# Performance work log

Hardware: AMD Instinct MI355X
Metric: run time of the kernel (lower is better)

The kernel has to match this reference:

```python
import jax, jax.numpy as jnp
import numpy as np

TAGSET = 64
START_TAG = 62
STOP_TAG = 63
B, S = 32, 256


def setup_inputs() -> dict:
    key = jax.random.key(0)
    k1, k2, k3 = jax.random.split(key, 3)
    features = jax.random.normal(k1, (B, S, TAGSET, TAGSET), dtype=jnp.float32)
    targets = jax.random.randint(k2, (B, S), 0, TAGSET * TAGSET, dtype=jnp.int64)
    lengths = jax.random.randint(k3, (B,), 1, S + 1, dtype=jnp.int64)
    # pack_padded_sequence requires lengths sorted descending; ensure max length = S
    lengths = jnp.sort(lengths)[::-1].at[0].set(S)
    return {"features": features, "targets": targets, "lengths": lengths}


def reference(features, targets, lengths):
    Bc, Sc, T, _ = features.shape
    # --- gold score: gather the score of the true (from_tag, to_tag) pair per token ---
    flat = features.reshape(Bc, Sc, T * T)                       # [B,S,T*T]
    scores_at_targets = jnp.take_along_axis(flat, targets[:, :, None], axis=2)[..., 0]
    valid = (jnp.arange(Sc)[None, :] < lengths[:, None])          # [B,S] pad mask
    gold_score = jnp.sum(jnp.where(valid, scores_at_targets, 0.0))

    # --- CRF forward algorithm (log-sum-exp recurrence over time) ---
    init = features[:, 0, START_TAG, :]                           # [B,T] (all lengths >= 1)
    feats_t = jnp.swapaxes(features, 0, 1)[1:]                    # [S-1,B,T,T]
    active = (jnp.arange(1, Sc)[:, None] < lengths[None, :])       # [S-1,B]

    def step(scores, inp):
        feat, act = inp                                           # feat [B,T,T], act [B]
        new = jax.nn.logsumexp(feat + scores[:, :, None], axis=1)  # lse over from-tag
        scores = jnp.where(act[:, None], new, scores)
        return scores, None

    scores_upto_t, _ = jax.lax.scan(step, init, (feats_t, active))
    all_paths_scores = jnp.sum(scores_upto_t[:, STOP_TAG])

    return (all_paths_scores - gold_score) / Bc
```

## Files before the change

### kernel.cpp

```cpp
#include <hip/hip_runtime.h>
#include <cmath>

#define NB 32
#define NS 256
#define NT 64
#define START_TAG 62
#define STOP_TAG 63
#define CL 8
#define NCH 32
#define GS 8.0f
#define LOG64 4.1588830833596715f
#define SP 66

typedef __attribute__((ext_vector_type(8))) short short8;
typedef __attribute__((ext_vector_type(4))) float float4v;

union FragU { unsigned u[4]; short8 s; };

__device__ inline unsigned short f2bf(float x) {
  unsigned u = __float_as_uint(x);
  u += 0x7fffu + ((u >> 16) & 1u);
  return (unsigned short)(u >> 16);
}
__device__ inline unsigned pack2(float a, float b) {
  return (unsigned)f2bf(a) | ((unsigned)f2bf(b) << 16);
}

__global__ __launch_bounds__(256) void chunk_kernel(
    const float* __restrict__ feat, const int* __restrict__ lengths,
    unsigned int* __restrict__ cmat) {
  const int b = blockIdx.x;
  const int c = blockIdx.y;
  const int len = lengths[b];
  const int t1 = 1 + c * CL;
  const int nmat = min(len, t1 + CL) - t1;
  if (nmat <= 0) return;

  __shared__ unsigned short Pb[2][NT * SP];
  __shared__ unsigned short Et[2][NT * SP];

  const int tid = threadIdx.x;
  const float* fb = feat + ((size_t)b * NS + t1) * (NT * NT);

  {
    const int cj = tid & 15, rk = tid >> 4;
    #pragma unroll
    for (int r = 0; r < 4; ++r) {
      const int row = rk + 16 * r;
      float4 f4 = *(const float4*)(fb + row * NT + 4 * cj);
      unsigned* dst = (unsigned*)&Pb[0][row * SP + 4 * cj];
      dst[0] = pack2(__expf(f4.x - GS), __expf(f4.y - GS));
      dst[1] = pack2(__expf(f4.z - GS), __expf(f4.w - GS));
    }
  }

  const int sj = tid & 15, r0 = tid >> 4;
  float4 raw[2][4];
  if (nmat > 1) {
    const float* p = fb + (NT * NT);
    raw[1][0] = *(const float4*)(p + (2 * r0     ) * NT + 4 * sj);
    raw[1][1] = *(const float4*)(p + (2 * r0 +  1) * NT + 4 * sj);
    raw[1][2] = *(const float4*)(p + (2 * r0 + 32) * NT + 4 * sj);
    raw[1][3] = *(const float4*)(p + (2 * r0 + 33) * NT + 4 * sj);
  }
  __syncthreads();

  const int lane = tid & 63, wv = tid >> 6;
  const int ln = lane & 15, q = lane >> 4;
  const int m0 = 16 * wv;
  int pp = 0;

  for (int k = 1; k < nmat; ++k) {
    const int pf = k & 1;
    if (k + 1 < nmat) {
      const float* p = fb + (size_t)(k + 1) * (NT * NT);
      raw[1 - pf][0] = *(const float4*)(p + (2 * r0     ) * NT + 4 * sj);
      raw[1 - pf][1] = *(const float4*)(p + (2 * r0 +  1) * NT + 4 * sj);
      raw[1 - pf][2] = *(const float4*)(p + (2 * r0 + 32) * NT + 4 * sj);
      raw[1 - pf][3] = *(const float4*)(p + (2 * r0 + 33) * NT + 4 * sj);
    }
    {
      unsigned short* et = Et[pf];
      const float* r0p = (const float*)&raw[pf][0];
      const float* r1p = (const float*)&raw[pf][1];
      const float* r2p = (const float*)&raw[pf][2];
      const float* r3p = (const float*)&raw[pf][3];
      #pragma unroll
      for (int cc = 0; cc < 4; ++cc) {
        const int j = 4 * sj + cc;
        *(unsigned*)&et[j * SP + 2 * r0] =
            pack2(__expf(r0p[cc] - GS), __expf(r1p[cc] - GS));
        *(unsigned*)&et[j * SP + 2 * r0 + 32] =
            pack2(__expf(r2p[cc] - GS), __expf(r3p[cc] - GS));
      }
    }
    __syncthreads();

    FragU a0, a1;
    const unsigned* ap = (const unsigned*)&Pb[pp][(m0 + ln) * SP];
    a0.u[0] = ap[4 * q + 0]; a0.u[1] = ap[4 * q + 1];
    a0.u[2] = ap[4 * q + 2]; a0.u[3] = ap[4 * q + 3];
    a1.u[0] = ap[16 + 4 * q + 0]; a1.u[1] = ap[16 + 4 * q + 1];
    a1.u[2] = ap[16 + 4 * q + 2]; a1.u[3] = ap[16 + 4 * q + 3];

    float4v acc[4];
    #pragma unroll
    for (int tc = 0; tc < 4; ++tc) {
      FragU b0, b1;
      const unsigned* bp = (const unsigned*)&Et[pf][(16 * tc + ln) * SP];
      b0.u[0] = bp[4 * q + 0]; b0.u[1] = bp[4 * q + 1];
      b0.u[2] = bp[4 * q + 2]; b0.u[3] = bp[4 * q + 3];
      b1.u[0] = bp[16 + 4 * q + 0]; b1.u[1] = bp[16 + 4 * q + 1];
      b1.u[2] = bp[16 + 4 * q + 2]; b1.u[3] = bp[16 + 4 * q + 3];
      float4v z = {0.f, 0.f, 0.f, 0.f};
      acc[tc] = __builtin_amdgcn_mfma_f32_16x16x32_bf16(a0.s, b0.s, z, 0, 0, 0);
      acc[tc] = __builtin_amdgcn_mfma_f32_16x16x32_bf16(a1.s, b1.s, acc[tc], 0, 0, 0);
    }

    unsigned short* pn = Pb[1 - pp];
    #pragma unroll
    for (int tc = 0; tc < 4; ++tc) {
      #pragma unroll
      for (int rg = 0; rg < 4; ++rg) {
        const int row = m0 + 4 * q + rg;
        pn[row * SP + 16 * tc + ln] = f2bf(acc[tc][rg] * 0.015625f);
      }
    }
    pp ^= 1;
  }
  __syncthreads();

  {
    const int j = tid >> 2, cg = tid & 3;
    unsigned ub[8];
    #pragma unroll
    for (int u = 0; u < 8; ++u) {
      unsigned short lo = Pb[pp][(16 * cg + 2 * u    ) * SP + j];
      unsigned short hi = Pb[pp][(16 * cg + 2 * u + 1) * SP + j];
      ub[u] = (unsigned)lo | ((unsigned)hi << 16);
    }
    unsigned* dst = cmat + ((size_t)b * NCH + c) * 2048 + j * 32 + cg * 8;
    *(uint4*)dst       = make_uint4(ub[0], ub[1], ub[2], ub[3]);
    *((uint4*)dst + 1) = make_uint4(ub[4], ub[5], ub[6], ub[7]);
  }
}

__global__ __launch_bounds__(64) void combine_kernel(
    const float* __restrict__ feat, const int* __restrict__ targets,
    const int* __restrict__ lengths, const unsigned int* __restrict__ cmat,
    float* __restrict__ out) {
  const int b = blockIdx.x;
  const int j = threadIdx.x;
  __shared__ float sv[NT];
  const int len = lengths[b];
  const float* f0 = feat + (size_t)b * NS * (NT * NT);

  float gold = 0.f;
  #pragma unroll
  for (int g = 0; g < 4; ++g) {
    const int s = j + 64 * g;
    if (s < len) {
      const int tgt = targets[b * NS + s];
      gold += f0[(size_t)s * (NT * NT) + tgt];
    }
  }

  float x = f0[START_TAG * NT + j];
  float m = x;
  #pragma unroll
  for (int off = 32; off; off >>= 1) m = fmaxf(m, __shfl_xor(m, off));
  float v = __expf(x - m);
  float L = m;

  const int nch = (len - 1 + CL - 1) / CL;
  uint4 Q0[8];
  if (nch > 0) {
    const uint4* P = (const uint4*)cmat + (size_t)b * NCH * 512 + j * 8;
    #pragma unroll
    for (int w = 0; w < 8; ++w) Q0[w] = P[w];
  }

  for (int c2 = 0; c2 < nch; ++c2) {
    sv[j] = v;
    __builtin_amdgcn_wave_barrier();

    uint4 Q1[8];
    if (c2 + 1 < nch) {
      const uint4* P = (const uint4*)cmat + ((size_t)b * NCH + c2 + 1) * 512 + j * 8;
      #pragma unroll
      for (int w = 0; w < 8; ++w) Q1[w] = P[w];
    }

    float acc = 0.f;
    const float4* svp = (const float4*)sv;
    #pragma unroll
    for (int w = 0; w < 8; ++w) {
      uint4 qq = Q0[w];
      float4 s0 = svp[2 * w], s1 = svp[2 * w + 1];
      acc = fmaf(__uint_as_float(qq.x << 16), s0.x, acc);
      acc = fmaf(__uint_as_float(qq.x & 0xffff0000u), s0.y, acc);
      acc = fmaf(__uint_as_float(qq.y << 16), s0.z, acc);
      acc = fmaf(__uint_as_float(qq.y & 0xffff0000u), s0.w, acc);
      acc = fmaf(__uint_as_float(qq.z << 16), s1.x, acc);
      acc = fmaf(__uint_as_float(qq.z & 0xffff0000u), s1.y, acc);
      acc = fmaf(__uint_as_float(qq.w << 16), s1.z, acc);
      acc = fmaf(__uint_as_float(qq.w & 0xffff0000u), s1.w, acc);
    }
    __builtin_amdgcn_wave_barrier();

    const int tt1 = 1 + c2 * CL;
    const int nmat = min(len, tt1 + CL) - tt1;
    L += (float)nmat * GS + (float)(nmat - 1) * LOG64;

    float mm = acc;
    #pragma unroll
    for (int off = 32; off; off >>= 1) mm = fmaxf(mm, __shfl_xor(mm, off));
    v = acc / mm;
    L += __logf(mm);

    #pragma unroll
    for (int w = 0; w < 8; ++w) Q0[w] = Q1[w];
  }

  float lv = __logf(v);
  float path = L + __shfl(lv, STOP_TAG);

  #pragma unroll
  for (int off = 32; off; off >>= 1) gold += __shfl_down(gold, off);
  if (j == 0) atomicAdd(out, (path - gold) * (1.0f / (float)NB));
}

extern "C" void kernel_launch(void* const* d_in, const int* in_sizes, int n_in,
                              void* d_out, int out_size, void* d_ws, size_t ws_size,
                              hipStream_t stream) {
  const float* feat    = (const float*)d_in[0];
  const int*   targets = (const int*)d_in[1];
  const int*   lengths = (const int*)d_in[2];
  unsigned int* cmat = (unsigned int*)d_ws;
  float* out = (float*)d_out;

  hipMemsetAsync(d_out, 0, sizeof(float), stream);
  chunk_kernel<<<dim3(NB, NCH), 256, 0, stream>>>(feat, lengths, cmat);
  combine_kernel<<<NB, 64, 0, stream>>>(feat, targets, lengths, cmat, out);
}
```

Before: 240.9 us.

## Compute each chunk product in one wave with register-resident MFMA fragments

Each chunk of the CRF transfer-matrix product now runs on a single 64-lane wave instead of a 256-thread block. The running product stays in MFMA B-fragment registers and is re-laid out with lane shuffles, which removes the shared-memory staging and block-wide barriers. Incoming feature tiles are read with strided scalar loads straight into A-fragment order, and the 1/64 scale is folded into the exponent. The combine kernel's dot product is split over four independent accumulators to shorten the FMA dependency chain. The costs are uncoalesced global loads, many shuffles, higher register pressure, and a simpler round-to-nearest bf16 conversion that no longer breaks ties to even.

```diff
diff --git a/kernel.cpp b/kernel.cpp
--- a/kernel.cpp
+++ b/kernel.cpp
@@ -10,139 +10,135 @@
 #define NCH 32
 #define GS 8.0f
 #define LOG64 4.1588830833596715f
-#define SP 66
 
 typedef __attribute__((ext_vector_type(8))) short short8;
 typedef __attribute__((ext_vector_type(4))) float float4v;
 
-union FragU { unsigned u[4]; short8 s; };
-
-__device__ inline unsigned short f2bf(float x) {
-  unsigned u = __float_as_uint(x);
-  u += 0x7fffu + ((u >> 16) & 1u);
-  return (unsigned short)(u >> 16);
-}
-__device__ inline unsigned pack2(float a, float b) {
-  return (unsigned)f2bf(a) | ((unsigned)f2bf(b) << 16);
+union FragU { unsigned u[4]; short8 s; unsigned short h[8]; };
+
+__device__ inline unsigned pkbf(float a, float b) {
+  unsigned ua = (__float_as_uint(a) + 0x8000u) >> 16;
+  unsigned ub = (__float_as_uint(b) + 0x8000u) & 0xffff0000u;
+  return ua | ub;
 }
 
 __global__ __launch_bounds__(256) void chunk_kernel(
     const float* __restrict__ feat, const int* __restrict__ lengths,
-    unsigned int* __restrict__ cmat) {
-  const int b = blockIdx.x;
-  const int c = blockIdx.y;
+    unsigned short* __restrict__ cmat) {
+  const int wv  = threadIdx.x >> 6;
+  const int gid = blockIdx.x * 4 + wv;
+  const int b   = gid >> 5;
+  const int c   = gid & 31;
   const int len = lengths[b];
-  const int t1 = 1 + c * CL;
+  const int t1  = 1 + c * CL;
   const int nmat = min(len, t1 + CL) - t1;
   if (nmat <= 0) return;
 
-  __shared__ unsigned short Pb[2][NT * SP];
-  __shared__ unsigned short Et[2][NT * SP];
-
-  const int tid = threadIdx.x;
+  const int lane = threadIdx.x & 63;
+  const int q  = lane >> 4;
+  const int cc = lane & 15;
+
   const float* fb = feat + ((size_t)b * NS + t1) * (NT * NT);
 
-  {
-    const int cj = tid & 15, rk = tid >> 4;
-    #pragma unroll
-    for (int r = 0; r < 4; ++r) {
-      const int row = rk + 16 * r;
-      float4 f4 = *(const float4*)(fb + row * NT + 4 * cj);
-      unsigned* dst = (unsigned*)&Pb[0][row * SP + 4 * cj];
-      dst[0] = pack2(__expf(f4.x - GS), __expf(f4.y - GS));
-      dst[1] = pack2(__expf(f4.z - GS), __expf(f4.w - GS));
-    }
-  }
-
-  const int sj = tid & 15, r0 = tid >> 4;
-  float4 raw[2][4];
+  FragU BQ[2][4];
+  #pragma unroll
+  for (int h = 0; h < 2; ++h)
+    #pragma unroll
+    for (int tj = 0; tj < 4; ++tj) {
+      const float* p = fb + (16 * tj + cc) * NT + 32 * h + 8 * q;
+      float4 x = *(const float4*)p;
+      float4 y = *(const float4*)(p + 4);
+      BQ[h][tj].u[0] = pkbf(__expf(x.x - GS), __expf(x.y - GS));
+      BQ[h][tj].u[1] = pkbf(__expf(x.z - GS), __expf(x.w - GS));
+      BQ[h][tj].u[2] = pkbf(__expf(y.x - GS), __expf(y.y - GS));
+      BQ[h][tj].u[3] = pkbf(__expf(y.z - GS), __expf(y.w - GS));
+    }
+
+  float raw[4][2][8];
   if (nmat > 1) {
-    const float* p = fb + (NT * NT);
-    raw[1][0] = *(const float4*)(p + (2 * r0     ) * NT + 4 * sj);
-    raw[1][1] = *(const float4*)(p + (2 * r0 +  1) * NT + 4 * sj);
-    raw[1][2] = *(const float4*)(p + (2 * r0 + 32) * NT + 4 * sj);
-    raw[1][3] = *(const float4*)(p + (2 * r0 + 33) * NT + 4 * sj);
-  }
-  __syncthreads();
-
-  const int lane = tid & 63, wv = tid >> 6;
-  const int ln = lane & 15, q = lane >> 4;
-  const int m0 = 16 * wv;
-  int pp = 0;
+    const float* p = fb + NT * NT;
+    #pragma unroll
+    for (int mi = 0; mi < 4; ++mi)
+      #pragma unroll
+      for (int kh = 0; kh < 2; ++kh)
+        #pragma unroll
+        for (int j = 0; j < 8; ++j)
+          raw[mi][kh][j] = p[(32 * kh + 8 * q + j) * NT + 16 * mi + cc];
+  }
+
+  const int src0 = (((q & 1) * 2) << 4) | cc;
+  const int src1 = src0 + 16;
+  const bool hi = (q >> 1) != 0;
 
   for (int k = 1; k < nmat; ++k) {
-    const int pf = k & 1;
+    FragU FA[4][2];
+    #pragma unroll
+    for (int mi = 0; mi < 4; ++mi)
+      #pragma unroll
+      for (int kh = 0; kh < 2; ++kh)
+        #pragma unroll
+        for (int j2 = 0; j2 < 4; ++j2)
+          FA[mi][kh].u[j2] =
+              pkbf(__expf(raw[mi][kh][2 * j2]     - (GS + LOG64)),
+                   __expf(raw[mi][kh][2 * j2 + 1] - (GS + LOG64)));
+
     if (k + 1 < nmat) {
       const float* p = fb + (size_t)(k + 1) * (NT * NT);
-      raw[1 - pf][0] = *(const float4*)(p + (2 * r0     ) * NT + 4 * sj);
-      raw[1 - pf][1] = *(const float4*)(p + (2 * r0 +  1) * NT + 4 * sj);
-      raw[1 - pf][2] = *(const float4*)(p + (2 * r0 + 32) * NT + 4 * sj);
-      raw[1 - pf][3] = *(const float4*)(p + (2 * r0 + 33) * NT + 4 * sj);
-    }
-    {
-      unsigned short* et = Et[pf];
-      const float* r0p = (const float*)&raw[pf][0];
-      const float* r1p = (const float*)&raw[pf][1];
-      const float* r2p = (const float*)&raw[pf][2];
-      const float* r3p = (const float*)&raw[pf][3];
-      #pragma unroll
-      for (int cc = 0; cc < 4; ++cc) {
-        const int j = 4 * sj + cc;
-        *(unsigned*)&et[j * SP + 2 * r0] =
-            pack2(__expf(r0p[cc] - GS), __expf(r1p[cc] - GS));
-        *(unsigned*)&et[j * SP + 2 * r0 + 32] =
-            pack2(__expf(r2p[cc] - GS), __expf(r3p[cc] - GS));
+      #pragma unroll
+      for (int mi = 0; mi < 4; ++mi)
+        #pragma unroll
+        for (int kh = 0; kh < 2; ++kh)
+          #pragma unroll
+          for (int j = 0; j < 8; ++j)
+            raw[mi][kh][j] = p[(32 * kh + 8 * q + j) * NT + 16 * mi + cc];
+    }
+
+    float4v acc[4][4];
+    #pragma unroll
+    for (int ti = 0; ti < 4; ++ti)
+      #pragma unroll
+      for (int tj = 0; tj < 4; ++tj) {
+        float4v z = {0.f, 0.f, 0.f, 0.f};
+        z = __builtin_amdgcn_mfma_f32_16x16x32_bf16(FA[ti][0].s, BQ[0][tj].s, z, 0, 0, 0);
+        acc[ti][tj] = __builtin_amdgcn_mfma_f32_16x16x32_bf16(FA[ti][1].s, BQ[1][tj].s, z, 0, 0, 0);
       }
-    }
-    __syncthreads();
-
-    FragU a0, a1;
-    const unsigned* ap = (const unsigned*)&Pb[pp][(m0 + ln) * SP];
-    a0.u[0] = ap[4 * q + 0]; a0.u[1] = ap[4 * q + 1];
-    a0.u[2] = ap[4 * q + 2]; a0.u[3] = ap[4 * q + 3];
-    a1.u[0] = ap[16 + 4 * q + 0]; a1.u[1] = ap[16 + 4 * q + 1];
-    a1.u[2] = ap[16 + 4 * q + 2]; a1.u[3] = ap[16 + 4 * q + 3];
-
-    float4v acc[4];
-    #pragma unroll
-    for (int tc = 0; tc < 4; ++tc) {
-      FragU b0, b1;
-      const unsigned* bp = (const unsigned*)&Et[pf][(16 * tc + ln) * SP];
-      b0.u[0] = bp[4 * q + 0]; b0.u[1] = bp[4 * q + 1];
-      b0.u[2] = bp[4 * q + 2]; b0.u[3] = bp[4 * q + 3];
-      b1.u[0] = bp[16 + 4 * q + 0]; b1.u[1] = bp[16 + 4 * q + 1];
-      b1.u[2] = bp[16 + 4 * q + 2]; b1.u[3] = bp[16 + 4 * q + 3];
-      float4v z = {0.f, 0.f, 0.f, 0.f};
-      acc[tc] = __builtin_amdgcn_mfma_f32_16x16x32_bf16(a0.s, b0.s, z, 0, 0, 0);
-      acc[tc] = __builtin_amdgcn_mfma_f32_16x16x32_bf16(a1.s, b1.s, acc[tc], 0, 0, 0);
-    }
-
-    unsigned short* pn = Pb[1 - pp];
-    #pragma unroll
-    for (int tc = 0; tc < 4; ++tc) {
-      #pragma unroll
-      for (int rg = 0; rg < 4; ++rg) {
-        const int row = m0 + 4 * q + rg;
-        pn[row * SP + 16 * tc + ln] = f2bf(acc[tc][rg] * 0.015625f);
+
+    unsigned pk01[4][4], pk23[4][4];
+    #pragma unroll
+    for (int ti = 0; ti < 4; ++ti)
+      #pragma unroll
+      for (int tj = 0; tj < 4; ++tj) {
+        pk01[ti][tj] = pkbf(acc[ti][tj][0], acc[ti][tj][1]);
+        pk23[ti][tj] = pkbf(acc[ti][tj][2], acc[ti][tj][3]);
       }
-    }
-    pp ^= 1;
-  }
-  __syncthreads();
-
-  {
-    const int j = tid >> 2, cg = tid & 3;
-    unsigned ub[8];
-    #pragma unroll
-    for (int u = 0; u < 8; ++u) {
-      unsigned short lo = Pb[pp][(16 * cg + 2 * u    ) * SP + j];
-      unsigned short hi = Pb[pp][(16 * cg + 2 * u + 1) * SP + j];
-      ub[u] = (unsigned)lo | ((unsigned)hi << 16);
-    }
-    unsigned* dst = cmat + ((size_t)b * NCH + c) * 2048 + j * 32 + cg * 8;
-    *(uint4*)dst       = make_uint4(ub[0], ub[1], ub[2], ub[3]);
-    *((uint4*)dst + 1) = make_uint4(ub[4], ub[5], ub[6], ub[7]);
-  }
+
+    #pragma unroll
+    for (int h = 0; h < 2; ++h)
+      #pragma unroll
+      for (int tj = 0; tj < 4; ++tj) {
+        unsigned a0 = (unsigned)__shfl((int)pk01[2 * h][tj],     src0);
+        unsigned b0 = (unsigned)__shfl((int)pk01[2 * h + 1][tj], src0);
+        unsigned a1 = (unsigned)__shfl((int)pk23[2 * h][tj],     src0);
+        unsigned b1 = (unsigned)__shfl((int)pk23[2 * h + 1][tj], src0);
+        unsigned a2 = (unsigned)__shfl((int)pk01[2 * h][tj],     src1);
+        unsigned b2 = (unsigned)__shfl((int)pk01[2 * h + 1][tj], src1);
+        unsigned a3 = (unsigned)__shfl((int)pk23[2 * h][tj],     src1);
+        unsigned b3 = (unsigned)__shfl((int)pk23[2 * h + 1][tj], src1);
+        BQ[h][tj].u[0] = hi ? b0 : a0;
+        BQ[h][tj].u[1] = hi ? b1 : a1;
+        BQ[h][tj].u[2] = hi ? b2 : a2;
+        BQ[h][tj].u[3] = hi ? b3 : a3;
+      }
+  }
+
+  unsigned short* dst = cmat + ((size_t)b * NCH + c) * (NT * NT);
+  #pragma unroll
+  for (int h = 0; h < 2; ++h)
+    #pragma unroll
+    for (int tj = 0; tj < 4; ++tj)
+      #pragma unroll
+      for (int j = 0; j < 8; ++j)
+        dst[(32 * h + 8 * q + j) * NT + 16 * tj + cc] = BQ[h][tj].h[j];
 }
 
 __global__ __launch_bounds__(64) void combine_kernel(
@@ -191,21 +187,22 @@
       for (int w = 0; w < 8; ++w) Q1[w] = P[w];
     }
 
-    float acc = 0.f;
+    float ac0 = 0.f, ac1 = 0.f, ac2 = 0.f, ac3 = 0.f;
     const float4* svp = (const float4*)sv;
     #pragma unroll
     for (int w = 0; w < 8; ++w) {
       uint4 qq = Q0[w];
       float4 s0 = svp[2 * w], s1 = svp[2 * w + 1];
-      acc = fmaf(__uint_as_float(qq.x << 16), s0.x, acc);
-      acc = fmaf(__uint_as_float(qq.x & 0xffff0000u), s0.y, acc);
-      acc = fmaf(__uint_as_float(qq.y << 16), s0.z, acc);
-      acc = fmaf(__uint_as_float(qq.y & 0xffff0000u), s0.w, acc);
-      acc = fmaf(__uint_as_float(qq.z << 16), s1.x, acc);
-      acc = fmaf(__uint_as_float(qq.z & 0xffff0000u), s1.y, acc);
-      acc = fmaf(__uint_as_float(qq.w << 16), s1.z, acc);
-      acc = fmaf(__uint_as_float(qq.w & 0xffff0000u), s1.w, acc);
-    }
+      ac0 = fmaf(__uint_as_float(qq.x << 16), s0.x, ac0);
+      ac1 = fmaf(__uint_as_float(qq.x & 0xffff0000u), s0.y, ac1);
+      ac2 = fmaf(__uint_as_float(qq.y << 16), s0.z, ac2);
+      ac3 = fmaf(__uint_as_float(qq.y & 0xffff0000u), s0.w, ac3);
+      ac0 = fmaf(__uint_as_float(qq.z << 16), s1.x, ac0);
+      ac1 = fmaf(__uint_as_float(qq.z & 0xffff0000u), s1.y, ac1);
+      ac2 = fmaf(__uint_as_float(qq.w << 16), s1.z, ac2);
+      ac3 = fmaf(__uint_as_float(qq.w & 0xffff0000u), s1.w, ac3);
+    }
+    float acc = (ac0 + ac1) + (ac2 + ac3);
     __builtin_amdgcn_wave_barrier();
 
     const int tt1 = 1 + c2 * CL;
@@ -236,10 +233,11 @@
   const float* feat    = (const float*)d_in[0];
   const int*   targets = (const int*)d_in[1];
   const int*   lengths = (const int*)d_in[2];
-  unsigned int* cmat = (unsigned int*)d_ws;
+  unsigned short* cmat = (unsigned short*)d_ws;
   float* out = (float*)d_out;
 
   hipMemsetAsync(d_out, 0, sizeof(float), stream);
-  chunk_kernel<<<dim3(NB, NCH), 256, 0, stream>>>(feat, lengths, cmat);
-  combine_kernel<<<NB, 64, 0, stream>>>(feat, targets, lengths, cmat, out);
-}
+  chunk_kernel<<<NB * NCH / 4, 256, 0, stream>>>(feat, lengths, cmat);
+  combine_kernel<<<NB, 64, 0, stream>>>(feat, targets, lengths,
+                                        (const unsigned int*)cmat, out);
+}
```

Result: faster. 223.4 us (-7.3%).
